# Performance work log

Measured on AMD Instinct MI355X. Metric: run time of the kernel, lower is better.

## Reference

```python
import jax, jax.numpy as jnp
import numpy as np

N = 32768        # atoms
INV = 256        # irreps_in[inv_field].dim (scalar latent width)
MUL = 32         # input eq multiplicity: '32x1o'
VOUT = 4         # output eq multiplicity: '4x1o'
HID = 512        # ScalarMLPFunction latent dims [512, 512]
INV_OUT = 2      # inv_out_irreps '2x0e'
TYPES = 32       # num_types
EPS = 1e-10


def _mlp(x, w1, w2, w3):
    # ScalarMLPFunction: Linear(+1/sqrt(fan_in) norm) -> SiLU -> ... -> Linear
    h = jax.nn.silu((x @ w1) * (1.0 / np.sqrt(w1.shape[0])))
    h = jax.nn.silu((h @ w2) * (1.0 / np.sqrt(w2.shape[0])))
    return (h @ w3) * (1.0 / np.sqrt(w3.shape[0]))


def setup_inputs() -> dict:
    key = jax.random.key(0)
    ks = jax.random.split(key, 10)
    inv_features = jax.random.normal(ks[0], (N, INV), dtype=jnp.float32)
    eq_features = jax.random.normal(ks[1], (N, MUL, 3), dtype=jnp.float32)
    atom_types = jax.random.randint(ks[2], (N, 1), 0, TYPES, dtype=jnp.int32)
    # hypernetwork (final_latent): INV -> 512 -> 512 -> MUL*VOUT
    w1_lat = jax.random.normal(ks[3], (INV, HID), dtype=jnp.float32)
    w2_lat = jax.random.normal(ks[4], (HID, HID), dtype=jnp.float32)
    w3_lat = jax.random.normal(ks[5], (HID, MUL * VOUT), dtype=jnp.float32)
    # final_readout: INV -> 512 -> 512 -> INV_OUT
    w1_ro = jax.random.normal(ks[6], (INV, HID), dtype=jnp.float32)
    w2_ro = jax.random.normal(ks[7], (HID, HID), dtype=jnp.float32)
    w3_ro = jax.random.normal(ks[8], (HID, INV_OUT), dtype=jnp.float32)
    # atom_type2bond_lengths parameter, init to ones as in the module
    bond_lengths = jnp.ones((TYPES, VOUT, 1), dtype=jnp.float32)
    return dict(inv_features=inv_features, eq_features=eq_features,
                atom_types=atom_types, w1_lat=w1_lat, w2_lat=w2_lat,
                w3_lat=w3_lat, w1_ro=w1_ro, w2_ro=w2_ro, w3_ro=w3_ro,
                bond_lengths=bond_lengths)


def reference(inv_features, eq_features, atom_types, w1_lat, w2_lat, w3_lat,
              w1_ro, w2_ro, w3_ro, bond_lengths):
    # hypernet-generated per-atom weights for the equivariant Linear
    weights = _mlp(inv_features, w1_lat, w2_lat, w3_lat)          # [N, MUL*VOUT]
    weights = weights.reshape(-1, MUL, VOUT)                      # [N, u, v]
    inv_out = _mlp(inv_features, w1_ro, w2_ro, w3_ro)             # [N, INV_OUT]
    # e3nn Linear '32x1o -> 4x1o', shared_weights=False, path norm 1/sqrt(mul_in)
    eq = jnp.einsum('num,nuv->nvm', eq_features, weights) * (1.0 / np.sqrt(MUL))
    # norm -> divide -> nan_to_num
    norm = jnp.linalg.norm(eq, axis=-1, keepdims=True)            # [N, VOUT, 1]
    eq = jnp.nan_to_num(eq / (norm + EPS), nan=0.0)
    # per-atom-type bond-length scale (gather-multiply)
    eq = eq * bond_lengths[atom_types[:, 0]]                      # [N, VOUT, 3]
    return inv_out, eq
```

## Files before the change

kernel.cpp:

```cpp
#include <hip/hip_runtime.h>
#include <hip/hip_bf16.h>

#define N_ATOMS 32768

typedef __attribute__((ext_vector_type(4))) float f32x4;
typedef __attribute__((ext_vector_type(8))) short bf16x8;
typedef unsigned short u16;

__device__ __forceinline__ u16 f2b(float f) {
    union { __hip_bfloat16 b; u16 u; } c;
    c.b = __float2bfloat16(f);
    return c.u;
}
__device__ __forceinline__ float b2f(u16 u) {
    union { unsigned int i; float f; } c;
    c.i = ((unsigned int)u) << 16;
    return c.f;
}

#define GLDS16(src, dst) __builtin_amdgcn_global_load_lds( \
    (const __attribute__((address_space(1))) void*)(src),  \
    (__attribute__((address_space(3))) void*)(dst), 16, 0, 0)


__global__ void convx_kernel(const float* __restrict__ x,
                             u16* __restrict__ xhi, u16* __restrict__ xlo) {
    size_t i = (size_t)(blockIdx.x * 256 + threadIdx.x) * 8;
    float4 v0 = *(const float4*)(x + i);
    float4 v1 = *(const float4*)(x + i + 4);
    float v[8] = {v0.x, v0.y, v0.z, v0.w, v1.x, v1.y, v1.z, v1.w};
    bf16x8 rh, rl;
#pragma unroll
    for (int j = 0; j < 8; ++j) {
        u16 h = f2b(v[j]);
        rh[j] = (short)h;
        rl[j] = (short)f2b(v[j] - b2f(h));
    }
    *(bf16x8*)(xhi + i) = rh;
    *(bf16x8*)(xlo + i) = rl;
}

__global__ void convw_kernel(const float* __restrict__ w1l, const float* __restrict__ w2l,
                             const float* __restrict__ w3l, const float* __restrict__ w1r,
                             const float* __restrict__ w2r,
                             u16* __restrict__ W1LThi, u16* __restrict__ W1LTlo,
                             u16* __restrict__ W1RT,
                             u16* __restrict__ W2LThi, u16* __restrict__ W2LTlo,
                             u16* __restrict__ W2RT,
                             u16* __restrict__ W3LThi, u16* __restrict__ W3LTlo) {
    int i = blockIdx.x * 256 + threadIdx.x;
    if (i < 131072) {
        int n = i >> 8, k = i & 255;
        float v = w1l[k * 512 + n];
        u16 h = f2b(v);
        W1LThi[i] = h;
        W1LTlo[i] = f2b(v - b2f(h));
    } else if (i < 262144) {
        int j = i - 131072;
        int n = j >> 8, k = j & 255;
        W1RT[j] = f2b(w1r[k * 512 + n]);
    } else if (i < 524288) {
        int j = i - 262144;
        int n = j >> 9, k = j & 511;
        float v = w2l[k * 512 + n];
        u16 h = f2b(v);
        W2LThi[j] = h;
        W2LTlo[j] = f2b(v - b2f(h));
    } else if (i < 786432) {
        int j = i - 524288;
        int n = j >> 9, k = j & 511;
        W2RT[j] = f2b(w2r[k * 512 + n]);
    } else if (i < 851968) {
        int j = i - 786432;
        int n = j >> 9, k = j & 511;
        float v = w3l[k * 128 + n];
        u16 h = f2b(v);
        W3LThi[j] = h;
        W3LTlo[j] = f2b(v - b2f(h));
    }
}

__global__ void zero_kernel(float* __restrict__ p) {
    int i = blockIdx.x * 256 + threadIdx.x;
    *(float4*)(p + i * 4) = float4{0.f, 0.f, 0.f, 0.f};
}

template<int NSEG, int GX, int NF, bool SILU, int OUTK>
__global__ void __launch_bounds__(512, 2) gemm8p(
        const u16* __restrict__ Ahi, const u16* __restrict__ Alo,
        const u16* __restrict__ Bhi, const u16* __restrict__ Blo,
        void* __restrict__ Chi, void* __restrict__ Clo,
        int ldc, int K, float scale,
        const float* __restrict__ e_w3, float* __restrict__ e_out) {
    constexpr int LBSZ = NF * 64 * 64;
    constexpr int SMEMN = 32768 + 2 * LBSZ;
    __shared__ __align__(16) u16 smem[SMEMN];
    u16* const lA0 = smem;
    u16* const lB0 = smem + 32768;
    const int tid = threadIdx.x;
    const int lane = tid & 63;
    const int wid = tid >> 6;
    const int wm = wid >> 2;
    const int wn = wid & 3;
    const int rlane = lane & 15;
    const int kc = lane >> 4;
    const int cps = rlane & 7;
    const int srow = tid >> 3;
    const int scp = tid & 7;

    const int nwg = gridDim.x;
    const int bid = blockIdx.x;
    const int wg = (bid & 7) * (nwg >> 3) + (bid >> 3);
    const int bn = (wg % GX) * (NF * 64);
    const int bm = (wg / GX) * 256;

    const int kt = K >> 6;
    const int NT = NSEG * kt;

    auto stageA = [&](int t, int buf) {
        int seg = (NSEG == 1) ? 0 : ((t >= kt) + (t >= 2 * kt));
        const u16* As = (NSEG == 1) ? Ahi : (seg == 1 ? Alo : Ahi);
        int k0 = (t - seg * kt) << 6;
        u16* la = lA0 + buf * 16384;
#pragma unroll
        for (int call = 0; call < 4; ++call) {
            int row = call * 64 + srow;
            int c = scp ^ (row & 7);
            GLDS16(As + (size_t)(bm + row) * K + k0 + c * 8, la + (size_t)(row * 64 + scp * 8));
        }
    };
    auto stageB = [&](int t, int buf) {
        int seg = (NSEG == 1) ? 0 : ((t >= kt) + (t >= 2 * kt));
        const u16* Bs = (NSEG == 1) ? Bhi : (seg == 2 ? Blo : Bhi);
        int k0 = (t - seg * kt) << 6;
        u16* lb = lB0 + buf * LBSZ;
#pragma unroll
        for (int call = 0; call < NF; ++call) {
            int row = call * 64 + srow;
            int c = scp ^ (row & 7);
            GLDS16(Bs + (size_t)(bn + row) * K + k0 + c * 8, lb + (size_t)(row * 64 + scp * 8));
        }
    };

    f32x4 acc[8][NF] = {};

    stageA(0, 0);
    stageB(0, 0);
    asm volatile("s_waitcnt vmcnt(0)" ::: "memory");
    __builtin_amdgcn_s_barrier();

    for (int t = 0; t < NT; ++t) {
        const int cur = t & 1, nxt = cur ^ 1;
        const bool pf = (t + 1 < NT);
        const u16* la = lA0 + cur * 16384;
        const u16* lb = lB0 + cur * LBSZ;
#pragma unroll
        for (int ks = 0; ks < 2; ++ks) {
            bf16x8 af[8], bfr[NF];
            const int cp = (ks * 4 + kc) ^ cps;
#pragma unroll
            for (int m = 0; m < 8; ++m) {
                int row = wm * 128 + m * 16 + rlane;
                af[m] = *(const bf16x8*)&la[row * 64 + cp * 8];
            }
#pragma unroll
            for (int n = 0; n < NF; ++n) {
                int row = wn * (NF * 16) + n * 16 + rlane;
                bfr[n] = *(const bf16x8*)&lb[row * 64 + cp * 8];
            }
            if (pf) {
                if (ks == 0) stageA(t + 1, nxt);
                else         stageB(t + 1, nxt);
            }
            asm volatile("s_waitcnt lgkmcnt(0)" ::: "memory");
            __builtin_amdgcn_sched_barrier(0);
            __builtin_amdgcn_s_setprio(1);
#pragma unroll
            for (int m = 0; m < 8; ++m)
#pragma unroll
                for (int n = 0; n < NF; ++n)
                    acc[m][n] = __builtin_amdgcn_mfma_f32_16x16x32_bf16(af[m], bfr[n], acc[m][n], 0, 0, 0);
            __builtin_amdgcn_s_setprio(0);
        }
        asm volatile("s_waitcnt vmcnt(0)" ::: "memory");
        __builtin_amdgcn_s_barrier();
    }

    const int g = lane >> 4;

    if constexpr (OUTK == 3) {
        const float s512f = 0.04419417382415922f;
        float wj0[NF], wj1[NF];
#pragma unroll
        for (int n = 0; n < NF; ++n) {
            int gc = bn + wn * (NF * 16) + n * 16 + rlane;
            wj0[n] = e_w3[gc * 2] * s512f;
            wj1[n] = e_w3[gc * 2 + 1] * s512f;
        }
#pragma unroll
        for (int m = 0; m < 8; ++m)
#pragma unroll
            for (int r = 0; r < 4; ++r) {
                float s0 = 0.f, s1 = 0.f;
#pragma unroll
                for (int n = 0; n < NF; ++n) {
                    float v = acc[m][n][r] * scale;
                    v = v / (1.0f + __expf(-v));
                    s0 = fmaf(v, wj0[n], s0);
                    s1 = fmaf(v, wj1[n], s1);
                }
#pragma unroll
                for (int off = 1; off < 16; off <<= 1) {
                    s0 += __shfl_xor(s0, off);
                    s1 += __shfl_xor(s1, off);
                }
                if (rlane == 0) {
                    int row = bm + wm * 128 + m * 16 + g * 4 + r;
                    atomicAdd(&e_out[row * 2], s0);
                    atomicAdd(&e_out[row * 2 + 1], s1);
                }
            }
        return;
    } else {
#pragma unroll
        for (int m = 0; m < 8; ++m) {
            int grow0 = bm + wm * 128 + m * 16 + (g << 2);
#pragma unroll
            for (int n = 0; n < NF; ++n) {
                int gcol = bn + wn * (NF * 16) + n * 16 + rlane;
#pragma unroll
                for (int r = 0; r < 4; ++r) {
                    float v = acc[m][n][r] * scale;
                    if constexpr (SILU) v = v / (1.0f + __expf(-v));
                    size_t idx = (size_t)(grow0 + r) * ldc + gcol;
                    if constexpr (OUTK == 0) {
                        ((float*)Chi)[idx] = v;
                    } else if constexpr (OUTK == 1) {
                        ((u16*)Chi)[idx] = f2b(v);
                    } else {
                        u16 h = f2b(v);
                        ((u16*)Chi)[idx] = h;
                        ((u16*)Clo)[idx] = f2b(v - b2f(h));
                    }
                }
            }
        }
    }
}

__global__ void eq_kernel(const float* __restrict__ eqf, const float* __restrict__ wgt,
                          const int* __restrict__ types, const float* __restrict__ bond,
                          float* __restrict__ out) {
    int t = blockIdx.x * 256 + threadIdx.x;
    int n = t >> 2, v = t & 3;
    const float* e = eqf + (size_t)n * 96;
    const float* w = wgt + (size_t)n * 128 + v;
    float a0 = 0.f, a1 = 0.f, a2 = 0.f;
#pragma unroll
    for (int u = 0; u < 32; ++u) {
        float wv = w[u * 4];
        a0 = fmaf(e[u * 3 + 0], wv, a0);
        a1 = fmaf(e[u * 3 + 1], wv, a1);
        a2 = fmaf(e[u * 3 + 2], wv, a2);
    }
    const float s = 0.17677669529663687f;
    a0 *= s; a1 *= s; a2 *= s;
    float norm = sqrtf(a0 * a0 + a1 * a1 + a2 * a2) + 1e-10f;
    float bl = bond[types[n] * 4 + v];
    float r0 = a0 / norm, r1 = a1 / norm, r2 = a2 / norm;
    if (isnan(r0)) r0 = 0.f;
    if (isnan(r1)) r1 = 0.f;
    if (isnan(r2)) r2 = 0.f;
    out[(size_t)n * 12 + v * 3 + 0] = r0 * bl;
    out[(size_t)n * 12 + v * 3 + 1] = r1 * bl;
    out[(size_t)n * 12 + v * 3 + 2] = r2 * bl;
}

extern "C" void kernel_launch(void* const* d_in, const int* in_sizes, int n_in,
                              void* d_out, int out_size, void* d_ws, size_t ws_size,
                              hipStream_t stream) {
    const float* inv  = (const float*)d_in[0];
    const float* eqf  = (const float*)d_in[1];
    const int*   typs = (const int*)d_in[2];
    const float* w1l  = (const float*)d_in[3];
    const float* w2l  = (const float*)d_in[4];
    const float* w3l  = (const float*)d_in[5];
    const float* w1r  = (const float*)d_in[6];
    const float* w2r  = (const float*)d_in[7];
    const float* w3r  = (const float*)d_in[8];
    const float* bond = (const float*)d_in[9];

    char* ws = (char*)d_ws;
    const size_t MB = 1024 * 1024, KB = 1024;
    u16* XHI   = (u16*)(ws);
    u16* XLO   = (u16*)(ws + 16 * MB);
    u16* H1R   = (u16*)(ws + 32 * MB);
    u16* H1Lhi = (u16*)(ws + 64 * MB);
    u16* H1Llo = (u16*)(ws + 96 * MB);
    u16* H2Lhi = (u16*)(ws);
    u16* H2Llo = (u16*)(ws + 32 * MB);
    float* WGT = (float*)(ws + 64 * MB);
    char* wb = ws + 160 * MB;
    u16* W1LThi = (u16*)(wb);
    u16* W1LTlo = (u16*)(wb + 256 * KB);
    u16* W1RT   = (u16*)(wb + 512 * KB);
    u16* W2LThi = (u16*)(wb + 768 * KB);
    u16* W2LTlo = (u16*)(wb + 1280 * KB);
    u16* W2RT   = (u16*)(wb + 1792 * KB);
    u16* W3LThi = (u16*)(wb + 2304 * KB);
    u16* W3LTlo = (u16*)(wb + 2432 * KB);

    float* out_inv = (float*)d_out;
    float* out_eq  = (float*)d_out + N_ATOMS * 2;

    const float s256 = 0.0625f;
    const float s512 = 0.04419417382415922f;

    convx_kernel<<<dim3(4096), dim3(256), 0, stream>>>(inv, XHI, XLO);
    convw_kernel<<<dim3(3328), dim3(256), 0, stream>>>(w1l, w2l, w3l, w1r, w2r,
        W1LThi, W1LTlo, W1RT, W2LThi, W2LTlo, W2RT, W3LThi, W3LTlo);
    zero_kernel<<<dim3(64), dim3(256), 0, stream>>>(out_inv);

    gemm8p<3, 2, 4, true, 2><<<dim3(256), dim3(512), 0, stream>>>(
        XHI, XLO, W1LThi, W1LTlo, H1Lhi, H1Llo, 512, 256, s256, nullptr, nullptr);
    gemm8p<1, 2, 4, true, 1><<<dim3(256), dim3(512), 0, stream>>>(
        XHI, nullptr, W1RT, nullptr, H1R, nullptr, 512, 256, s256, nullptr, nullptr);
    gemm8p<1, 2, 4, true, 3><<<dim3(256), dim3(512), 0, stream>>>(
        H1R, nullptr, W2RT, nullptr, nullptr, nullptr, 0, 512, s512, w3r, out_inv);
    gemm8p<3, 2, 4, true, 2><<<dim3(256), dim3(512), 0, stream>>>(
        H1Lhi, H1Llo, W2LThi, W2LTlo, H2Lhi, H2Llo, 512, 512, s512, nullptr, nullptr);
    gemm8p<3, 2, 1, false, 0><<<dim3(256), dim3(512), 0, stream>>>(
        H2Lhi, H2Llo, W3LThi, W3LTlo, WGT, nullptr, 128, 512, s512, nullptr, nullptr);
    eq_kernel<<<dim3(512), dim3(256), 0, stream>>>(eqf, WGT, typs, bond, out_eq);
}
```

Baseline: 196.5 us.

## Merge setup kernels and co-launch independent latent and readout GEMMs

Folds the three preprocessing kernels (input split, weight transpose/split, output zeroing) into one launch. It also pairs the independent latent-branch and readout-branch GEMMs of each layer into a single grid of 512 blocks, dispatched by block index. This cuts launch count and lets the two branches fill the GPU at the same time instead of running back to back. Workspace offsets are moved so the concurrently written buffers do not alias. The cost is a shared LDS allocation sized for the larger variant, and possible imbalance between the 3-pass and 1-pass halves of each grid.

```diff
diff --git a/kernel.cpp b/kernel.cpp
--- a/kernel.cpp
+++ b/kernel.cpp
@@ -22,79 +22,77 @@
     (const __attribute__((address_space(1))) void*)(src),  \
     (__attribute__((address_space(3))) void*)(dst), 16, 0, 0)
 
-
-__global__ void convx_kernel(const float* __restrict__ x,
-                             u16* __restrict__ xhi, u16* __restrict__ xlo) {
-    size_t i = (size_t)(blockIdx.x * 256 + threadIdx.x) * 8;
-    float4 v0 = *(const float4*)(x + i);
-    float4 v1 = *(const float4*)(x + i + 4);
-    float v[8] = {v0.x, v0.y, v0.z, v0.w, v1.x, v1.y, v1.z, v1.w};
-    bf16x8 rh, rl;
-#pragma unroll
-    for (int j = 0; j < 8; ++j) {
-        u16 h = f2b(v[j]);
-        rh[j] = (short)h;
-        rl[j] = (short)f2b(v[j] - b2f(h));
+__global__ void __launch_bounds__(256) setup_kernel(
+        const float* __restrict__ x, u16* __restrict__ xhi, u16* __restrict__ xlo,
+        const float* __restrict__ w1l, const float* __restrict__ w2l,
+        const float* __restrict__ w3l, const float* __restrict__ w1r,
+        const float* __restrict__ w2r,
+        u16* __restrict__ W1LThi, u16* __restrict__ W1LTlo, u16* __restrict__ W1RT,
+        u16* __restrict__ W2LThi, u16* __restrict__ W2LTlo, u16* __restrict__ W2RT,
+        u16* __restrict__ W3LThi, u16* __restrict__ W3LTlo,
+        float* __restrict__ out_inv) {
+    int bid = blockIdx.x;
+    if (bid < 4096) {
+        size_t i = (size_t)(bid * 256 + threadIdx.x) * 8;
+        float4 v0 = *(const float4*)(x + i);
+        float4 v1 = *(const float4*)(x + i + 4);
+        float v[8] = {v0.x, v0.y, v0.z, v0.w, v1.x, v1.y, v1.z, v1.w};
+        bf16x8 rh, rl;
+#pragma unroll
+        for (int j = 0; j < 8; ++j) {
+            u16 h = f2b(v[j]);
+            rh[j] = (short)h;
+            rl[j] = (short)f2b(v[j] - b2f(h));
+        }
+        *(bf16x8*)(xhi + i) = rh;
+        *(bf16x8*)(xlo + i) = rl;
+    } else if (bid < 7424) {
+        int i = (bid - 4096) * 256 + threadIdx.x;
+        if (i < 131072) {
+            int n = i >> 8, k = i & 255;
+            float v = w1l[k * 512 + n];
+            u16 h = f2b(v);
+            W1LThi[i] = h;
+            W1LTlo[i] = f2b(v - b2f(h));
+        } else if (i < 262144) {
+            int j = i - 131072;
+            int n = j >> 8, k = j & 255;
+            W1RT[j] = f2b(w1r[k * 512 + n]);
+        } else if (i < 524288) {
+            int j = i - 262144;
+            int n = j >> 9, k = j & 511;
+            float v = w2l[k * 512 + n];
+            u16 h = f2b(v);
+            W2LThi[j] = h;
+            W2LTlo[j] = f2b(v - b2f(h));
+        } else if (i < 786432) {
+            int j = i - 524288;
+            int n = j >> 9, k = j & 511;
+            W2RT[j] = f2b(w2r[k * 512 + n]);
+        } else if (i < 851968) {
+            int j = i - 786432;
+            int n = j >> 9, k = j & 511;
+            float v = w3l[k * 128 + n];
+            u16 h = f2b(v);
+            W3LThi[j] = h;
+            W3LTlo[j] = f2b(v - b2f(h));
+        }
+    } else {
+        int i = (bid - 7424) * 256 + threadIdx.x;
+        *(float4*)(out_inv + i * 4) = float4{0.f, 0.f, 0.f, 0.f};
     }
-    *(bf16x8*)(xhi + i) = rh;
-    *(bf16x8*)(xlo + i) = rl;
-}
-
-__global__ void convw_kernel(const float* __restrict__ w1l, const float* __restrict__ w2l,
-                             const float* __restrict__ w3l, const float* __restrict__ w1r,
-                             const float* __restrict__ w2r,
-                             u16* __restrict__ W1LThi, u16* __restrict__ W1LTlo,
-                             u16* __restrict__ W1RT,
-                             u16* __restrict__ W2LThi, u16* __restrict__ W2LTlo,
-                             u16* __restrict__ W2RT,
-                             u16* __restrict__ W3LThi, u16* __restrict__ W3LTlo) {
-    int i = blockIdx.x * 256 + threadIdx.x;
-    if (i < 131072) {
-        int n = i >> 8, k = i & 255;
-        float v = w1l[k * 512 + n];
-        u16 h = f2b(v);
-        W1LThi[i] = h;
-        W1LTlo[i] = f2b(v - b2f(h));
-    } else if (i < 262144) {
-        int j = i - 131072;
-        int n = j >> 8, k = j & 255;
-        W1RT[j] = f2b(w1r[k * 512 + n]);
-    } else if (i < 524288) {
-        int j = i - 262144;
-        int n = j >> 9, k = j & 511;
-        float v = w2l[k * 512 + n];
-        u16 h = f2b(v);
-        W2LThi[j] = h;
-        W2LTlo[j] = f2b(v - b2f(h));
-    } else if (i < 786432) {
-        int j = i - 524288;
-        int n = j >> 9, k = j & 511;
-        W2RT[j] = f2b(w2r[k * 512 + n]);
-    } else if (i < 851968) {
-        int j = i - 786432;
-        int n = j >> 9, k = j & 511;
-        float v = w3l[k * 128 + n];
-        u16 h = f2b(v);
-        W3LThi[j] = h;
-        W3LTlo[j] = f2b(v - b2f(h));
-    }
-}
-
-__global__ void zero_kernel(float* __restrict__ p) {
-    int i = blockIdx.x * 256 + threadIdx.x;
-    *(float4*)(p + i * 4) = float4{0.f, 0.f, 0.f, 0.f};
-}
-
-template<int NSEG, int GX, int NF, bool SILU, int OUTK>
-__global__ void __launch_bounds__(512, 2) gemm8p(
+}
+
+template<int NSEG, int NF, bool SILU, int OUTK>
+__device__ __forceinline__ void gemm_body(
+        u16* __restrict__ smem,
         const u16* __restrict__ Ahi, const u16* __restrict__ Alo,
         const u16* __restrict__ Bhi, const u16* __restrict__ Blo,
         void* __restrict__ Chi, void* __restrict__ Clo,
         int ldc, int K, float scale,
-        const float* __restrict__ e_w3, float* __restrict__ e_out) {
+        const float* __restrict__ e_w3, float* __restrict__ e_out,
+        int bid, int nwg, int GX) {
     constexpr int LBSZ = NF * 64 * 64;
-    constexpr int SMEMN = 32768 + 2 * LBSZ;
-    __shared__ __align__(16) u16 smem[SMEMN];
     u16* const lA0 = smem;
     u16* const lB0 = smem + 32768;
     const int tid = threadIdx.x;
@@ -108,8 +106,6 @@
     const int srow = tid >> 3;
     const int scp = tid & 7;
 
-    const int nwg = gridDim.x;
-    const int bid = blockIdx.x;
     const int wg = (bid & 7) * (nwg >> 3) + (bid >> 3);
     const int bn = (wg % GX) * (NF * 64);
     const int bm = (wg / GX) * 256;
@@ -220,7 +216,6 @@
                     atomicAdd(&e_out[row * 2 + 1], s1);
                 }
             }
-        return;
     } else {
 #pragma unroll
         for (int m = 0; m < 8; ++m) {
@@ -246,6 +241,49 @@
             }
         }
     }
+}
+
+static constexpr float S256 = 0.0625f;
+static constexpr float S512 = 0.04419417382415922f;
+
+__global__ void __launch_bounds__(512, 2) gemm_l1(
+        const u16* __restrict__ XHI, const u16* __restrict__ XLO,
+        const u16* __restrict__ W1LThi, const u16* __restrict__ W1LTlo,
+        const u16* __restrict__ W1RT,
+        u16* __restrict__ H1Lhi, u16* __restrict__ H1Llo, u16* __restrict__ H1R) {
+    __shared__ __align__(16) u16 smem[65536];
+    int bid = blockIdx.x;
+    if (bid < 256)
+        gemm_body<3, 4, true, 2>(smem, XHI, XLO, W1LThi, W1LTlo, H1Lhi, H1Llo,
+                                 512, 256, S256, nullptr, nullptr, bid, 256, 2);
+    else
+        gemm_body<1, 4, true, 1>(smem, XHI, nullptr, W1RT, nullptr, H1R, nullptr,
+                                 512, 256, S256, nullptr, nullptr, bid - 256, 256, 2);
+}
+
+__global__ void __launch_bounds__(512, 2) gemm_l2(
+        const u16* __restrict__ H1Lhi, const u16* __restrict__ H1Llo,
+        const u16* __restrict__ W2LThi, const u16* __restrict__ W2LTlo,
+        const u16* __restrict__ H1R, const u16* __restrict__ W2RT,
+        u16* __restrict__ H2Lhi, u16* __restrict__ H2Llo,
+        const float* __restrict__ w3r, float* __restrict__ out_inv) {
+    __shared__ __align__(16) u16 smem[65536];
+    int bid = blockIdx.x;
+    if (bid < 256)
+        gemm_body<3, 4, true, 2>(smem, H1Lhi, H1Llo, W2LThi, W2LTlo, H2Lhi, H2Llo,
+                                 512, 512, S512, nullptr, nullptr, bid, 256, 2);
+    else
+        gemm_body<1, 4, true, 3>(smem, H1R, nullptr, W2RT, nullptr, nullptr, nullptr,
+                                 0, 512, S512, w3r, out_inv, bid - 256, 256, 2);
+}
+
+__global__ void __launch_bounds__(512, 2) gemm_l3(
+        const u16* __restrict__ H2Lhi, const u16* __restrict__ H2Llo,
+        const u16* __restrict__ W3LThi, const u16* __restrict__ W3LTlo,
+        float* __restrict__ WGT) {
+    __shared__ __align__(16) u16 smem[40960];
+    gemm_body<3, 1, false, 0>(smem, H2Lhi, H2Llo, W3LThi, W3LTlo, WGT, nullptr,
+                              128, 512, S512, nullptr, nullptr, (int)blockIdx.x, 256, 2);
 }
 
 __global__ void eq_kernel(const float* __restrict__ eqf, const float* __restrict__ wgt,
@@ -298,8 +336,8 @@
     u16* H1Lhi = (u16*)(ws + 64 * MB);
     u16* H1Llo = (u16*)(ws + 96 * MB);
     u16* H2Lhi = (u16*)(ws);
-    u16* H2Llo = (u16*)(ws + 32 * MB);
-    float* WGT = (float*)(ws + 64 * MB);
+    u16* H2Llo = (u16*)(ws + 128 * MB);
+    float* WGT = (float*)(ws + 32 * MB);
     char* wb = ws + 160 * MB;
     u16* W1LThi = (u16*)(wb);
     u16* W1LTlo = (u16*)(wb + 256 * KB);
@@ -313,23 +351,13 @@
     float* out_inv = (float*)d_out;
     float* out_eq  = (float*)d_out + N_ATOMS * 2;
 
-    const float s256 = 0.0625f;
-    const float s512 = 0.04419417382415922f;
-
-    convx_kernel<<<dim3(4096), dim3(256), 0, stream>>>(inv, XHI, XLO);
-    convw_kernel<<<dim3(3328), dim3(256), 0, stream>>>(w1l, w2l, w3l, w1r, w2r,
-        W1LThi, W1LTlo, W1RT, W2LThi, W2LTlo, W2RT, W3LThi, W3LTlo);
-    zero_kernel<<<dim3(64), dim3(256), 0, stream>>>(out_inv);
-
-    gemm8p<3, 2, 4, true, 2><<<dim3(256), dim3(512), 0, stream>>>(
-        XHI, XLO, W1LThi, W1LTlo, H1Lhi, H1Llo, 512, 256, s256, nullptr, nullptr);
-    gemm8p<1, 2, 4, true, 1><<<dim3(256), dim3(512), 0, stream>>>(
-        XHI, nullptr, W1RT, nullptr, H1R, nullptr, 512, 256, s256, nullptr, nullptr);
-    gemm8p<1, 2, 4, true, 3><<<dim3(256), dim3(512), 0, stream>>>(
-        H1R, nullptr, W2RT, nullptr, nullptr, nullptr, 0, 512, s512, w3r, out_inv);
-    gemm8p<3, 2, 4, true, 2><<<dim3(256), dim3(512), 0, stream>>>(
-        H1Lhi, H1Llo, W2LThi, W2LTlo, H2Lhi, H2Llo, 512, 512, s512, nullptr, nullptr);
-    gemm8p<3, 2, 1, false, 0><<<dim3(256), dim3(512), 0, stream>>>(
-        H2Lhi, H2Llo, W3LThi, W3LTlo, WGT, nullptr, 128, 512, s512, nullptr, nullptr);
+    setup_kernel<<<dim3(7488), dim3(256), 0, stream>>>(
+        inv, XHI, XLO, w1l, w2l, w3l, w1r, w2r,
+        W1LThi, W1LTlo, W1RT, W2LThi, W2LTlo, W2RT, W3LThi, W3LTlo, out_inv);
+    gemm_l1<<<dim3(512), dim3(512), 0, stream>>>(
+        XHI, XLO, W1LThi, W1LTlo, W1RT, H1Lhi, H1Llo, H1R);
+    gemm_l2<<<dim3(512), dim3(512), 0, stream>>>(
+        H1Lhi, H1Llo, W2LThi, W2LTlo, H1R, W2RT, H2Lhi, H2Llo, w3r, out_inv);
+    gemm_l3<<<dim3(256), dim3(512), 0, stream>>>(H2Lhi, H2Llo, W3LThi, W3LTlo, WGT);
     eq_kernel<<<dim3(512), dim3(256), 0, stream>>>(eqf, WGT, typs, bond, out_eq);
 }
```

Result: faster. 190.6 us (-3.0%).

## Add dedicated double-buffered split-bf16 GEMM kernel and merge setup kernels

Applied to the files above, without the earlier changes.

Introduces a new gemm4p kernel for the two 3-segment hi/lo latent-MLP layers. It stages A and B tiles into LDS with global_load_lds double buffering, issues split-K-half prefetches interleaved with MFMA blocks under setprio, and keeps one 512-thread block per CU. It also fuses the three setup kernels (x conversion, weight transpose/convert, output zeroing) into one launch to cut launch overhead, and relocates some workspace buffers. The new kernel uses 128KB of LDS with launch bound occupancy 1, which trades latency hiding via occupancy for explicit software pipelining.

```diff
diff --git a/kernel.cpp b/kernel.cpp
--- a/kernel.cpp
+++ b/kernel.cpp
@@ -22,67 +22,211 @@
     (const __attribute__((address_space(1))) void*)(src),  \
     (__attribute__((address_space(3))) void*)(dst), 16, 0, 0)
 
-
-__global__ void convx_kernel(const float* __restrict__ x,
-                             u16* __restrict__ xhi, u16* __restrict__ xlo) {
-    size_t i = (size_t)(blockIdx.x * 256 + threadIdx.x) * 8;
-    float4 v0 = *(const float4*)(x + i);
-    float4 v1 = *(const float4*)(x + i + 4);
-    float v[8] = {v0.x, v0.y, v0.z, v0.w, v1.x, v1.y, v1.z, v1.w};
-    bf16x8 rh, rl;
-#pragma unroll
-    for (int j = 0; j < 8; ++j) {
-        u16 h = f2b(v[j]);
-        rh[j] = (short)h;
-        rl[j] = (short)f2b(v[j] - b2f(h));
-    }
-    *(bf16x8*)(xhi + i) = rh;
-    *(bf16x8*)(xlo + i) = rl;
-}
-
-__global__ void convw_kernel(const float* __restrict__ w1l, const float* __restrict__ w2l,
-                             const float* __restrict__ w3l, const float* __restrict__ w1r,
-                             const float* __restrict__ w2r,
-                             u16* __restrict__ W1LThi, u16* __restrict__ W1LTlo,
-                             u16* __restrict__ W1RT,
-                             u16* __restrict__ W2LThi, u16* __restrict__ W2LTlo,
-                             u16* __restrict__ W2RT,
-                             u16* __restrict__ W3LThi, u16* __restrict__ W3LTlo) {
-    int i = blockIdx.x * 256 + threadIdx.x;
-    if (i < 131072) {
-        int n = i >> 8, k = i & 255;
-        float v = w1l[k * 512 + n];
-        u16 h = f2b(v);
-        W1LThi[i] = h;
-        W1LTlo[i] = f2b(v - b2f(h));
-    } else if (i < 262144) {
-        int j = i - 131072;
-        int n = j >> 8, k = j & 255;
-        W1RT[j] = f2b(w1r[k * 512 + n]);
-    } else if (i < 524288) {
-        int j = i - 262144;
-        int n = j >> 9, k = j & 511;
-        float v = w2l[k * 512 + n];
-        u16 h = f2b(v);
-        W2LThi[j] = h;
-        W2LTlo[j] = f2b(v - b2f(h));
-    } else if (i < 786432) {
-        int j = i - 524288;
-        int n = j >> 9, k = j & 511;
-        W2RT[j] = f2b(w2r[k * 512 + n]);
-    } else if (i < 851968) {
-        int j = i - 786432;
-        int n = j >> 9, k = j & 511;
-        float v = w3l[k * 128 + n];
-        u16 h = f2b(v);
-        W3LThi[j] = h;
-        W3LTlo[j] = f2b(v - b2f(h));
-    }
-}
-
-__global__ void zero_kernel(float* __restrict__ p) {
-    int i = blockIdx.x * 256 + threadIdx.x;
-    *(float4*)(p + i * 4) = float4{0.f, 0.f, 0.f, 0.f};
+__global__ void __launch_bounds__(256) setup_kernel(
+        const float* __restrict__ x, u16* __restrict__ xhi, u16* __restrict__ xlo,
+        const float* __restrict__ w1l, const float* __restrict__ w2l,
+        const float* __restrict__ w3l, const float* __restrict__ w1r,
+        const float* __restrict__ w2r,
+        u16* __restrict__ W1LThi, u16* __restrict__ W1LTlo, u16* __restrict__ W1RT,
+        u16* __restrict__ W2LThi, u16* __restrict__ W2LTlo, u16* __restrict__ W2RT,
+        u16* __restrict__ W3LThi, u16* __restrict__ W3LTlo,
+        float* __restrict__ out_inv) {
+    int bid = blockIdx.x;
+    if (bid < 4096) {
+        size_t i = (size_t)(bid * 256 + threadIdx.x) * 8;
+        float4 v0 = *(const float4*)(x + i);
+        float4 v1 = *(const float4*)(x + i + 4);
+        float v[8] = {v0.x, v0.y, v0.z, v0.w, v1.x, v1.y, v1.z, v1.w};
+        bf16x8 rh, rl;
+#pragma unroll
+        for (int j = 0; j < 8; ++j) {
+            u16 h = f2b(v[j]);
+            rh[j] = (short)h;
+            rl[j] = (short)f2b(v[j] - b2f(h));
+        }
+        *(bf16x8*)(xhi + i) = rh;
+        *(bf16x8*)(xlo + i) = rl;
+    } else if (bid < 7424) {
+        int i = (bid - 4096) * 256 + threadIdx.x;
+        if (i < 131072) {
+            int n = i >> 8, k = i & 255;
+            float v = w1l[k * 512 + n];
+            u16 h = f2b(v);
+            W1LThi[i] = h;
+            W1LTlo[i] = f2b(v - b2f(h));
+        } else if (i < 262144) {
+            int j = i - 131072;
+            int n = j >> 8, k = j & 255;
+            W1RT[j] = f2b(w1r[k * 512 + n]);
+        } else if (i < 524288) {
+            int j = i - 262144;
+            int n = j >> 9, k = j & 511;
+            float v = w2l[k * 512 + n];
+            u16 h = f2b(v);
+            W2LThi[j] = h;
+            W2LTlo[j] = f2b(v - b2f(h));
+        } else if (i < 786432) {
+            int j = i - 524288;
+            int n = j >> 9, k = j & 511;
+            W2RT[j] = f2b(w2r[k * 512 + n]);
+        } else if (i < 851968) {
+            int j = i - 786432;
+            int n = j >> 9, k = j & 511;
+            float v = w3l[k * 128 + n];
+            u16 h = f2b(v);
+            W3LThi[j] = h;
+            W3LTlo[j] = f2b(v - b2f(h));
+        }
+    } else {
+        int i = (bid - 7424) * 256 + threadIdx.x;
+        *(float4*)(out_inv + i * 4) = float4{0.f, 0.f, 0.f, 0.f};
+    }
+}
+
+template<int GX>
+__global__ void __launch_bounds__(512, 1) gemm4p(
+        const u16* __restrict__ Ahi, const u16* __restrict__ Alo,
+        const u16* __restrict__ Bhi, const u16* __restrict__ Blo,
+        u16* __restrict__ Chi, u16* __restrict__ Clo,
+        int ldc, int K, float scale) {
+    __shared__ __align__(16) u16 smem[65536];
+    u16* const lA0 = smem;
+    u16* const lB0 = smem + 32768;
+    const int tid = threadIdx.x;
+    const int lane = tid & 63;
+    const int wid = tid >> 6;
+    const int wm = wid >> 2;
+    const int wn = wid & 3;
+    const int rlane = lane & 15;
+    const int kc = lane >> 4;
+    const int srow0 = tid >> 2;
+    const int scp = tid & 3;
+
+    const int nwg = gridDim.x;
+    const int bid = blockIdx.x;
+    const int wg = (bid & 7) * (nwg >> 3) + (bid >> 3);
+    const int bn = (wg % GX) * 256;
+    const int bm = (wg / GX) * 256;
+
+    const int kt = K >> 6;
+    const int NT = 3 * kt;
+
+    auto stageA = [&](int t, int buf, int kh) {
+        int seg = (t >= kt) + (t >= 2 * kt);
+        const u16* As = (seg == 1) ? Alo : Ahi;
+        int k0 = (t - seg * kt) * 64 + kh * 32;
+        u16* la = lA0 + buf * 16384 + kh * 8192;
+#pragma unroll
+        for (int call = 0; call < 2; ++call) {
+            int row = call * 128 + srow0;
+            int c = scp ^ ((row >> 1) & 3);
+            GLDS16(As + (size_t)(bm + row) * K + k0 + c * 8, la + row * 32 + scp * 8);
+        }
+    };
+    auto stageB = [&](int t, int buf, int kh) {
+        int seg = (t >= kt) + (t >= 2 * kt);
+        const u16* Bs = (seg == 2) ? Blo : Bhi;
+        int k0 = (t - seg * kt) * 64 + kh * 32;
+        u16* lb = lB0 + buf * 16384 + kh * 8192;
+#pragma unroll
+        for (int call = 0; call < 2; ++call) {
+            int row = call * 128 + srow0;
+            int c = scp ^ ((row >> 1) & 3);
+            GLDS16(Bs + (size_t)(bn + row) * K + k0 + c * 8, lb + row * 32 + scp * 8);
+        }
+    };
+
+    f32x4 acc[8][4] = {};
+    bf16x8 af[4], bf[4];
+
+#define RD_A(buf, kh, mh) do {                                                \
+        const u16* la_ = lA0 + (buf) * 16384 + (kh) * 8192;                   \
+        _Pragma("unroll")                                                     \
+        for (int m_ = 0; m_ < 4; ++m_) {                                      \
+            int row_ = wm * 128 + (mh) * 64 + m_ * 16 + rlane;                \
+            int c_ = kc ^ ((row_ >> 1) & 3);                                  \
+            af[m_] = *(const bf16x8*)&la_[row_ * 32 + c_ * 8];                \
+        }                                                                     \
+    } while (0)
+#define RD_B(buf, kh) do {                                                    \
+        const u16* lb_ = lB0 + (buf) * 16384 + (kh) * 8192;                   \
+        _Pragma("unroll")                                                     \
+        for (int n_ = 0; n_ < 4; ++n_) {                                      \
+            int row_ = wn * 64 + n_ * 16 + rlane;                             \
+            int c_ = kc ^ ((row_ >> 1) & 3);                                  \
+            bf[n_] = *(const bf16x8*)&lb_[row_ * 32 + c_ * 8];                \
+        }                                                                     \
+    } while (0)
+#define LGKM0 do {                                                            \
+        asm volatile("s_waitcnt lgkmcnt(0)" ::: "memory");                    \
+        __builtin_amdgcn_sched_barrier(0);                                    \
+    } while (0)
+#define MM(mh) do {                                                           \
+        __builtin_amdgcn_s_setprio(1);                                        \
+        _Pragma("unroll")                                                     \
+        for (int m_ = 0; m_ < 4; ++m_)                                        \
+            _Pragma("unroll")                                                 \
+            for (int n_ = 0; n_ < 4; ++n_)                                    \
+                acc[(mh) * 4 + m_][n_] = __builtin_amdgcn_mfma_f32_16x16x32_bf16( \
+                    af[m_], bf[n_], acc[(mh) * 4 + m_][n_], 0, 0, 0);         \
+        __builtin_amdgcn_s_setprio(0);                                        \
+    } while (0)
+
+    stageA(0, 0, 0);
+    stageB(0, 0, 0);
+    stageA(0, 0, 1);
+    stageB(0, 0, 1);
+
+    for (int t = 0; t < NT; ++t) {
+        const int cur = t & 1, oth = cur ^ 1;
+        const bool pf = (t + 1 < NT);
+        asm volatile("s_waitcnt vmcnt(4)" ::: "memory");
+        __builtin_amdgcn_s_barrier();
+        RD_B(cur, 0);
+        RD_A(cur, 0, 0);
+        if (pf) stageA(t + 1, oth, 0);
+        LGKM0;
+        MM(0);
+        RD_A(cur, 0, 1);
+        if (pf) stageB(t + 1, oth, 0);
+        LGKM0;
+        MM(1);
+        if (pf) asm volatile("s_waitcnt vmcnt(4)" ::: "memory");
+        else    asm volatile("s_waitcnt vmcnt(0)" ::: "memory");
+        __builtin_amdgcn_s_barrier();
+        RD_B(cur, 1);
+        RD_A(cur, 1, 0);
+        if (pf) stageA(t + 1, oth, 1);
+        LGKM0;
+        MM(0);
+        RD_A(cur, 1, 1);
+        if (pf) stageB(t + 1, oth, 1);
+        LGKM0;
+        MM(1);
+    }
+#undef MM
+#undef LGKM0
+#undef RD_B
+#undef RD_A
+
+    const int g = lane >> 4;
+#pragma unroll
+    for (int m = 0; m < 8; ++m) {
+        int grow0 = bm + wm * 128 + m * 16 + (g << 2);
+#pragma unroll
+        for (int n = 0; n < 4; ++n) {
+            int gcol = bn + wn * 64 + n * 16 + rlane;
+#pragma unroll
+            for (int r = 0; r < 4; ++r) {
+                float v = acc[m][n][r] * scale;
+                v = v / (1.0f + __expf(-v));
+                size_t idx = (size_t)(grow0 + r) * ldc + gcol;
+                u16 h = f2b(v);
+                Chi[idx] = h;
+                Clo[idx] = f2b(v - b2f(h));
+            }
+        }
+    }
 }
 
 template<int NSEG, int GX, int NF, bool SILU, int OUTK>
@@ -220,7 +364,6 @@
                     atomicAdd(&e_out[row * 2 + 1], s1);
                 }
             }
-        return;
     } else {
 #pragma unroll
         for (int m = 0; m < 8; ++m) {
@@ -233,15 +376,8 @@
                     float v = acc[m][n][r] * scale;
                     if constexpr (SILU) v = v / (1.0f + __expf(-v));
                     size_t idx = (size_t)(grow0 + r) * ldc + gcol;
-                    if constexpr (OUTK == 0) {
-                        ((float*)Chi)[idx] = v;
-                    } else if constexpr (OUTK == 1) {
-                        ((u16*)Chi)[idx] = f2b(v);
-                    } else {
-                        u16 h = f2b(v);
-                        ((u16*)Chi)[idx] = h;
-                        ((u16*)Clo)[idx] = f2b(v - b2f(h));
-                    }
+                    if constexpr (OUTK == 0) ((float*)Chi)[idx] = v;
+                    else                     ((u16*)Chi)[idx] = f2b(v);
                 }
             }
         }
@@ -298,8 +434,8 @@
     u16* H1Lhi = (u16*)(ws + 64 * MB);
     u16* H1Llo = (u16*)(ws + 96 * MB);
     u16* H2Lhi = (u16*)(ws);
-    u16* H2Llo = (u16*)(ws + 32 * MB);
-    float* WGT = (float*)(ws + 64 * MB);
+    u16* H2Llo = (u16*)(ws + 128 * MB);
+    float* WGT = (float*)(ws + 32 * MB);
     char* wb = ws + 160 * MB;
     u16* W1LThi = (u16*)(wb);
     u16* W1LTlo = (u16*)(wb + 256 * KB);
@@ -316,19 +452,17 @@
     const float s256 = 0.0625f;
     const float s512 = 0.04419417382415922f;
 
-    convx_kernel<<<dim3(4096), dim3(256), 0, stream>>>(inv, XHI, XLO);
-    convw_kernel<<<dim3(3328), dim3(256), 0, stream>>>(w1l, w2l, w3l, w1r, w2r,
-        W1LThi, W1LTlo, W1RT, W2LThi, W2LTlo, W2RT, W3LThi, W3LTlo);
-    zero_kernel<<<dim3(64), dim3(256), 0, stream>>>(out_inv);
-
-    gemm8p<3, 2, 4, true, 2><<<dim3(256), dim3(512), 0, stream>>>(
-        XHI, XLO, W1LThi, W1LTlo, H1Lhi, H1Llo, 512, 256, s256, nullptr, nullptr);
+    setup_kernel<<<dim3(7488), dim3(256), 0, stream>>>(
+        inv, XHI, XLO, w1l, w2l, w3l, w1r, w2r,
+        W1LThi, W1LTlo, W1RT, W2LThi, W2LTlo, W2RT, W3LThi, W3LTlo, out_inv);
+    gemm4p<2><<<dim3(256), dim3(512), 0, stream>>>(
+        XHI, XLO, W1LThi, W1LTlo, H1Lhi, H1Llo, 512, 256, s256);
     gemm8p<1, 2, 4, true, 1><<<dim3(256), dim3(512), 0, stream>>>(
         XHI, nullptr, W1RT, nullptr, H1R, nullptr, 512, 256, s256, nullptr, nullptr);
     gemm8p<1, 2, 4, true, 3><<<dim3(256), dim3(512), 0, stream>>>(
         H1R, nullptr, W2RT, nullptr, nullptr, nullptr, 0, 512, s512, w3r, out_inv);
-    gemm8p<3, 2, 4, true, 2><<<dim3(256), dim3(512), 0, stream>>>(
-        H1Lhi, H1Llo, W2LThi, W2LTlo, H2Lhi, H2Llo, 512, 512, s512, nullptr, nullptr);
+    gemm4p<2><<<dim3(256), dim3(512), 0, stream>>>(
+        H1Lhi, H1Llo, W2LThi, W2LTlo, H2Lhi, H2Llo, 512, 512, s512);
     gemm8p<3, 2, 1, false, 0><<<dim3(256), dim3(512), 0, stream>>>(
         H2Lhi, H2Llo, W3LThi, W3LTlo, WGT, nullptr, 128, 512, s512, nullptr, nullptr);
     eq_kernel<<<dim3(512), dim3(256), 0, stream>>>(eqf, WGT, typs, bond, out_eq);
```

After: 196.4 us. No clear change (-0.1%).
